# Kernel tuning notes

Measured on AMD Instinct MI355X. Metric: run time of the kernel, lower is better.

## Reference

```python
import jax, jax.numpy as jnp
import numpy as np

MIN = 1e-30
BLOCK = 64


def setup_inputs() -> dict:
    key = jax.random.key(0)
    ks = jax.random.split(key, 16)
    B, L, D, H, M, E, P, R = 4, 512, 768, 12, 48, 32, 512, 97
    inp = {
        "context": jax.random.normal(ks[0], (B, L, D), jnp.float32),
        "attention": jax.random.uniform(ks[1], (B, H, L, L), jnp.float32),
        "mention_map": jax.random.uniform(ks[2], (B, M, L), jnp.float32),
        "entity_map": jax.random.uniform(ks[3], (B, E, M), jnp.float32),
        "hts": jax.random.randint(ks[4], (B, P, 2), 0, E).astype(jnp.int64),
        "hW": jax.random.normal(ks[5], (D, D), jnp.float32) * 0.02,
        "hb": jnp.zeros((D,), jnp.float32),
        "tW": jax.random.normal(ks[6], (D, D), jnp.float32) * 0.02,
        "tb": jnp.zeros((D,), jnp.float32),
        "hcW": jax.random.normal(ks[7], (D, D), jnp.float32) * 0.02,
        "hcb": jnp.zeros((D,), jnp.float32),
        "tcW": jax.random.normal(ks[8], (D, D), jnp.float32) * 0.02,
        "tcb": jnp.zeros((D,), jnp.float32),
        "clasW": jax.random.normal(ks[9], (R, D * BLOCK), jnp.float32) * 0.02,
        "clasb": jnp.zeros((R,), jnp.float32),
    }
    return inp


def _group_bilinear(h, t, W, b):
    # h, t: [B, P, D]; grouped bilinear a la ATLOP: block-outer-product then linear
    B, P, D = h.shape
    nb = D // BLOCK
    h_ = h.reshape(B, P, nb, BLOCK)
    t_ = t.reshape(B, P, nb, BLOCK)
    feat = jnp.einsum("bpni,bpnj->bpnij", h_, t_).reshape(B, P, D * BLOCK)
    return feat @ W.T + b


def _forward(context, attention, mention_map, entity_map, hts,
             hW, hb, tW, tb, hcW, hcb, tcW, tcb, clasW, clasb):
    B = context.shape[0]
    bidx = jnp.arange(B)[:, None]
    h_idx = hts[..., 0]  # [B, P]
    t_idx = hts[..., 1]
    ht_mask = (hts.sum(-1) != 0)[..., None].astype(context.dtype)  # [B, P, 1]

    # ---- get_ht ----
    mention = mention_map @ context                       # [B, M, D]
    att_sum = attention.sum(axis=1)                       # [B, L, L]
    mention_att = mention_map @ att_sum @ jnp.swapaxes(mention_map, 1, 2)  # [B, M, M]
    entity_att = entity_map @ mention_att                 # [B, E, M]

    h_mask = entity_map[bidx, h_idx] * ht_mask            # [B, P, M]
    t_mask = entity_map[bidx, t_idx] * ht_mask
    h_att = entity_att[bidx, h_idx] * t_mask
    t_att = entity_att[bidx, t_idx] * h_mask
    h_att = h_att / (h_att.sum(-1, keepdims=True) + MIN)
    t_att = t_att / (t_att.sum(-1, keepdims=True) + MIN)
    h = (t_att @ mention) * ht_mask                       # [B, P, D]
    t = (h_att @ mention) * ht_mask

    # ---- context_pooling (entity_map projected to token space) ----
    em_tok = entity_map @ mention_map                     # [B, E, L]
    em_tok = em_tok / (em_tok.sum(-1, keepdims=True) + MIN)
    ent_att = jnp.einsum("bel,bhlm->bhem", em_tok, attention)  # [B, H, E, L]
    hA = ent_att[bidx, :, h_idx]                          # [B, P, H, L]
    tA = ent_att[bidx, :, t_idx]
    ctx_att = (hA * tA).sum(axis=2)                       # [B, P, L]
    ctx_att = ctx_att / (ctx_att.sum(-1, keepdims=True) + MIN)
    context_info = (ctx_att @ context) * ht_mask          # [B, P, D]

    h_info = context_info @ hcW.T + hcb
    t_info = context_info @ tcW.T + tcb
    h = jnp.tanh(h @ hW.T + hb + h_info)
    t = jnp.tanh(t @ tW.T + tb + t_info)
    return _group_bilinear(h, t, clasW, clasb)            # [B, P, R]


def reference(context, attention, mention_map, entity_map, hts,
              hW, hb, tW, tb, hcW, hcb, tcW, tcb, clasW, clasb):
    return _forward(context, attention, mention_map, entity_map, hts,
                    hW, hb, tW, tb, hcW, hcb, tcW, tcb, clasW, clasb)
```

## Files before the change

### kernel.cpp

```cpp
#include <hip/hip_runtime.h>
#include <math.h>

#define Bc 4
#define Lc 512
#define Dc 768
#define Hc 12
#define Mc 48
#define Ec 32
#define Pc 512
#define Rc 97
#define MINV 1e-30f
#define NSLICE 24

typedef _Float16 f16;
typedef __attribute__((ext_vector_type(8))) _Float16 f16x8;
typedef __attribute__((ext_vector_type(4))) _Float16 f16x4;
typedef __attribute__((ext_vector_type(16))) float f32x16;

__global__ __launch_bounds__(256) void k_prep(const float* __restrict__ ctx, f16* __restrict__ ctxT,
                                              const float* __restrict__ mm, f16* __restrict__ mmH,
                                              const float* __restrict__ em, f16* __restrict__ emtH,
                                              float* __restrict__ tmpML) {
    __shared__ f16 Ts[64][72];
    __shared__ float rowS[Mc];
    __shared__ float red[256];
    __shared__ float inv;
    int bid = blockIdx.x;
    int tid = threadIdx.x;
    if (bid < 384) {
        int id = bid;
        int dt = id % 12; int lt = (id / 12) % 8; int b = id / 96;
        int l0 = lt * 64, d0 = dt * 64;
        int r = tid >> 2, cg = tid & 3;
        const float* src = ctx + ((size_t)b * Lc + l0 + r) * Dc + d0 + cg * 16;
#pragma unroll
        for (int u = 0; u < 4; ++u) {
            float4 v = ((const float4*)src)[u];
            Ts[cg * 16 + u * 4 + 0][r] = (f16)v.x;
            Ts[cg * 16 + u * 4 + 1][r] = (f16)v.y;
            Ts[cg * 16 + u * 4 + 2][r] = (f16)v.z;
            Ts[cg * 16 + u * 4 + 3][r] = (f16)v.w;
        }
        __syncthreads();
        int dr = tid >> 2, seg = tid & 3;
        f16* dst = ctxT + ((size_t)b * Dc + d0 + dr) * Lc + l0 + seg * 16;
        f16x8 o0, o1;
#pragma unroll
        for (int j = 0; j < 8; ++j) { o0[j] = Ts[dr][seg * 16 + j]; o1[j] = Ts[dr][seg * 16 + 8 + j]; }
        *(f16x8*)dst = o0;
        *(f16x8*)(dst + 8) = o1;
    } else if (bid < 432) {
        int gid = (bid - 384) * 256 + tid;
        const float4* src = (const float4*)(mm + (size_t)gid * 8);
        float4 v0 = src[0], v1 = src[1];
        f16x8 o;
        o[0] = (f16)v0.x; o[1] = (f16)v0.y; o[2] = (f16)v0.z; o[3] = (f16)v0.w;
        o[4] = (f16)v1.x; o[5] = (f16)v1.y; o[6] = (f16)v1.z; o[7] = (f16)v1.w;
        ((f16x8*)mmH)[gid] = o;
    } else if (bid < 560) {
        int be = bid - 432; int b = be / Ec;
        if (tid < Mc) rowS[tid] = em[(size_t)be * Mc + tid];
        __syncthreads();
        float v0 = 0.f, v1 = 0.f;
        {
            const float* mb0 = mm + (size_t)b * Mc * Lc + tid;
            const float* mb1 = mm + (size_t)b * Mc * Lc + tid + 256;
            for (int m = 0; m < Mc; ++m) {
                v0 += rowS[m] * mb0[(size_t)m * Lc];
                v1 += rowS[m] * mb1[(size_t)m * Lc];
            }
        }
        red[tid] = v0 + v1;
        __syncthreads();
        for (int s = 128; s > 0; s >>= 1) { if (tid < s) red[tid] += red[tid + s]; __syncthreads(); }
        if (tid == 0) inv = 1.f / (red[0] + MINV);
        __syncthreads();
        emtH[(size_t)be * Lc + tid] = (f16)(v0 * inv);
        emtH[(size_t)be * Lc + tid + 256] = (f16)(v1 * inv);
    } else {
        int base = ((bid - 560) * 256 + tid) * 4;
        float4 z = make_float4(0.f, 0.f, 0.f, 0.f);
        float4* t4 = (float4*)tmpML;
#pragma unroll
        for (int u = 0; u < 4; ++u) t4[base + u] = z;
    }
}

__global__ __launch_bounds__(256) void k_att_mention(const f16* __restrict__ mmH,
                                                     const f16* __restrict__ emtH,
                                                     const float* __restrict__ att,
                                                     float* __restrict__ tmpML,
                                                     float* __restrict__ eat,
                                                     const f16* __restrict__ ctxT,
                                                     float* __restrict__ mention,
                                                     const float* __restrict__ hW, const float* __restrict__ tW,
                                                     const float* __restrict__ hcW, const float* __restrict__ tcW,
                                                     f16* __restrict__ hWb, f16* __restrict__ tWb,
                                                     f16* __restrict__ hcWb, f16* __restrict__ tcWb,
                                                     const float* __restrict__ clasW, f16* __restrict__ Wp) {
    __shared__ __align__(16) char smem[32768];
    int bid = blockIdx.x;
    int tid = threadIdx.x;
    int w = tid >> 6, lane = tid & 63;
    if (bid < 384) {
        f16* Ss   = (f16*)smem;
        f16* attS = (f16*)(smem + 12288);
        int mt = bid & 7; int bh = bid >> 3;
        int b = bh / Hc, h = bh % Hc;
        int m0 = mt * 64;
        int n_l = lane & 31, kg = lane >> 5;

        const float* ab = att + (size_t)bh * Lc * Lc + m0;
        int mRow = tid & 63, lg = tid >> 6;
        float pre[16];
#pragma unroll
        for (int q = 0; q < 16; ++q) pre[q] = ab[(size_t)(lg * 16 + q) * Lc + mRow];

        f32x16 acc[2];
#pragma unroll
        for (int nt = 0; nt < 2; ++nt)
#pragma unroll
            for (int i = 0; i < 16; ++i) acc[nt][i] = 0.f;

        for (int kc = 0; kc < 8; ++kc) {
            __syncthreads();
#pragma unroll
            for (int half = 0; half < 2; ++half) {
                int cc = lg * 2 + half;
                f16x8 v;
#pragma unroll
                for (int jj = 0; jj < 8; ++jj) v[jj] = (f16)pre[half * 8 + jj];
                ((f16x8*)attS)[mRow * 8 + (cc ^ (mRow & 7))] = v;
            }
#pragma unroll
            for (int k = 0; k < 3; ++k) {
                int idx = tid + k * 256;
                int row = idx >> 3, cc = idx & 7;
                f16x8 v;
                if (row < Mc) {
                    v = *(const f16x8*)(mmH + ((size_t)b * Mc + row) * Lc + kc * 64 + cc * 8);
                } else if (row < 80) {
                    v = *(const f16x8*)(emtH + ((size_t)b * Ec + row - Mc) * Lc + kc * 64 + cc * 8);
                } else {
#pragma unroll
                    for (int j = 0; j < 8; ++j) v[j] = (f16)0.f;
                }
                ((f16x8*)Ss)[row * 8 + (cc ^ (row & 7))] = v;
            }
            if (kc < 7) {
#pragma unroll
                for (int q = 0; q < 16; ++q)
                    pre[q] = ab[(size_t)((kc + 1) * 64 + lg * 16 + q) * Lc + mRow];
            }
            __syncthreads();
            if (w < 3) {
                int arow = w * 32 + n_l;
#pragma unroll
                for (int kk = 0; kk < 4; ++kk) {
                    int cc = kk * 2 + kg;
                    f16x8 a = ((const f16x8*)Ss)[arow * 8 + (cc ^ (arow & 7))];
#pragma unroll
                    for (int nt = 0; nt < 2; ++nt) {
                        int bcol = nt * 32 + n_l;
                        f16x8 bb = ((const f16x8*)attS)[bcol * 8 + (cc ^ (bcol & 7))];
                        acc[nt] = __builtin_amdgcn_mfma_f32_32x32x16_f16(a, bb, acc[nt], 0, 0, 0);
                    }
                }
            }
        }
        if (w < 3) {
#pragma unroll
            for (int nt = 0; nt < 2; ++nt)
#pragma unroll
                for (int reg = 0; reg < 16; ++reg) {
                    int row = (reg & 3) + 8 * (reg >> 2) + 4 * kg;
                    int rr = w * 32 + row;
                    int col = m0 + nt * 32 + n_l;
                    if (rr < Mc) {
                        atomicAdd(&tmpML[((size_t)b * Mc + rr) * Lc + col], acc[nt][reg]);
                    } else if (rr < 80) {
                        eat[(((size_t)b * Hc + h) * Ec + (rr - Mc)) * Lc + col] = acc[nt][reg];
                    }
                }
        }
    } else if (bid < 432) {
        f16* As = (f16*)smem;
        f16* Bs = (f16*)(smem + 16384);
        int id = bid - 384;
        int dt = id % 12; int b = id / 12;
        int d0 = dt * 64;
        int w_m = w & 1, w_n = w >> 1;
        int m_l = lane & 31, kg = lane >> 5;
        int r0 = tid >> 3, cc0 = tid & 7;
        int r1 = r0 + 32;
        int mr0 = (r0 < Mc) ? r0 : r0 - Mc;
        int mr1 = (r1 < Mc) ? r1 : r1 - Mc;
        f16x8 ar0, ar1, br0, br1;
        auto loadt = [&](int it) {
            int k0 = it * 64;
            ar0 = *(const f16x8*)(mmH + ((size_t)b * Mc + mr0) * Lc + k0 + cc0 * 8);
            ar1 = *(const f16x8*)(mmH + ((size_t)b * Mc + mr1) * Lc + k0 + cc0 * 8);
            br0 = *(const f16x8*)(ctxT + ((size_t)b * Dc + d0 + r0) * Lc + k0 + cc0 * 8);
            br1 = *(const f16x8*)(ctxT + ((size_t)b * Dc + d0 + r1) * Lc + k0 + cc0 * 8);
        };
        auto writet = [&](int p) {
            ((f16x8*)(As + p * 4096))[r0 * 8 + (cc0 ^ (r0 & 7))] = ar0;
            ((f16x8*)(As + p * 4096))[r1 * 8 + (cc0 ^ (r1 & 7))] = ar1;
            ((f16x8*)(Bs + p * 4096))[r0 * 8 + (cc0 ^ (r0 & 7))] = br0;
            ((f16x8*)(Bs + p * 4096))[r1 * 8 + (cc0 ^ (r1 & 7))] = br1;
        };
        loadt(0); writet(0); loadt(1);
        f32x16 acc;
#pragma unroll
        for (int i = 0; i < 16; ++i) acc[i] = 0.f;
        int ar = w_m * 32 + m_l;
        int br = w_n * 32 + m_l;
        for (int it = 0; it < 8; ++it) {
            int p = it & 1;
            __syncthreads();
            if (it < 7) writet(p ^ 1);
            if (it < 6) loadt(it + 2);
#pragma unroll
            for (int s = 0; s < 4; ++s) {
                int ck = s * 2 + kg;
                f16x8 a = ((const f16x8*)(As + p * 4096))[ar * 8 + (ck ^ (ar & 7))];
                f16x8 bv = ((const f16x8*)(Bs + p * 4096))[br * 8 + (ck ^ (br & 7))];
                acc = __builtin_amdgcn_mfma_f32_32x32x16_f16(a, bv, acc, 0, 0, 0);
            }
        }
#pragma unroll
        for (int reg = 0; reg < 16; ++reg) {
            int row = (reg & 3) + 8 * (reg >> 2) + 4 * kg;
            int m = w_m * 32 + row;
            if (m < Mc) mention[((size_t)b * Mc + m) * Dc + d0 + w_n * 32 + m_l] = acc[reg];
        }
    } else if (bid < 2480) {
        const int Q = 147456;
        int i = (bid - 432) * 256 + tid;
        int stride = 2048 * 256;
        for (; i < 4 * Q; i += stride) {
            int sel = i / Q, j = i % Q;
            const float* s = (sel == 0) ? hW : (sel == 1) ? tW : (sel == 2) ? hcW : tcW;
            f16* d = (sel == 0) ? hWb : (sel == 1) ? tWb : (sel == 2) ? hcWb : tcWb;
            float4 v = ((const float4*)s)[j];
            f16x4 o;
            o[0] = (f16)v.x; o[1] = (f16)v.y; o[2] = (f16)v.z; o[3] = (f16)v.w;
            ((f16x4*)d)[j] = o;
        }
    } else {
        f16 (*LsW)[72] = (f16 (*)[72])smem;
        int id2 = bid - 2480;
        int c = id2 >> 2, rt = id2 & 3;
        for (int idx = tid; idx < 512; idx += 256) {
            int row = idx >> 4, q = idx & 15;
            int r = rt * 32 + row;
            f16x4 o;
            if (r < Rc) {
                float4 v = *(const float4*)(clasW + (size_t)r * (Dc * 64) + c * 64 + q * 4);
                o[0] = (f16)v.x; o[1] = (f16)v.y; o[2] = (f16)v.z; o[3] = (f16)v.w;
            } else {
                o[0] = (f16)0.f; o[1] = (f16)0.f; o[2] = (f16)0.f; o[3] = (f16)0.f;
            }
            *(f16x4*)(&LsW[row][q * 4]) = o;
        }
        __syncthreads();
        int s = tid >> 6;
        int n_l = lane & 31, kg = lane >> 5;
        f16x8 outv = *(const f16x8*)(&LsW[n_l][s * 16 + kg * 8]);
        ((f16x8*)Wp)[(size_t)(c * 16 + s * 4 + rt) * 64 + lane] = outv;
    }
}

__global__ __launch_bounds__(256) void k_ma(const float* __restrict__ tmp,
                                            const float* __restrict__ mm,
                                            float* __restrict__ maS) {
    int wv = threadIdx.x >> 6, lane = threadIdx.x & 63;
    int gid = blockIdx.x * 4 + wv;
    int m2 = gid % 48;
    int m  = (gid / 48) % 48;
    int b  = gid / (48 * 48);
    const float4* t = (const float4*)(tmp + ((size_t)b * Mc + m)  * Lc);
    const float4* r = (const float4*)(mm  + ((size_t)b * Mc + m2) * Lc);
    float4 a0 = t[lane],      b0 = r[lane];
    float4 a1 = t[lane + 64], b1 = r[lane + 64];
    float acc = a0.x * b0.x + a0.y * b0.y + a0.z * b0.z + a0.w * b0.w
              + a1.x * b1.x + a1.y * b1.y + a1.z * b1.z + a1.w * b1.w;
#pragma unroll
    for (int off = 1; off < 64; off <<= 1) acc += __shfl_xor(acc, off);
    if (lane == 0) maS[gid] = acc;
}

__global__ __launch_bounds__(256) void k_pair(const int* __restrict__ hts,
                                              const float* __restrict__ em,
                                              const float* __restrict__ maS,
                                              const float* __restrict__ eat,
                                              f16* __restrict__ hatN, f16* __restrict__ tatN,
                                              f16* __restrict__ caH) {
    int wv = threadIdx.x >> 6, lane = threadIdx.x & 63;
    int bp = blockIdx.x * 4 + wv;
    int b = bp >> 9;
    int hi = hts[bp * 2], ti = hts[bp * 2 + 1];
    float mask = (hi + ti != 0) ? 1.f : 0.f;
    float hat = 0.f, tat = 0.f;
    if (lane < Mc) {
        float hm = em[((size_t)(b * Ec + hi)) * Mc + lane];
        float tm = em[((size_t)(b * Ec + ti)) * Mc + lane];
        float eh = 0.f, et = 0.f;
        const float* maB = maS + (size_t)b * Mc * Mc;
        const float* emH = em + ((size_t)(b * Ec + hi)) * Mc;
        const float* emT = em + ((size_t)(b * Ec + ti)) * Mc;
#pragma unroll 8
        for (int m = 0; m < Mc; ++m) {
            float ms = maB[m * Mc + lane];
            eh += emH[m] * ms;
            et += emT[m] * ms;
        }
        hat = eh * tm * mask;
        tat = et * hm * mask;
    }
    float sh = hat, st = tat;
#pragma unroll
    for (int off = 1; off < 64; off <<= 1) { sh += __shfl_xor(sh, off); st += __shfl_xor(st, off); }
    float hnorm = 1.f / (sh + MINV);
    float tnorm = 1.f / (st + MINV);
    hatN[(size_t)bp * 64 + lane] = (f16)(hat * hnorm);
    tatN[(size_t)bp * 64 + lane] = (f16)(tat * tnorm);

    const float* base = eat + (size_t)b * Hc * Ec * Lc;
    float prod[8];
    float tot = 0.f;
#pragma unroll
    for (int j8 = 0; j8 < 8; ++j8) {
        int j = j8 * 64 + lane;
        float a = 0.f;
#pragma unroll
        for (int h = 0; h < Hc; ++h)
            a += base[((size_t)h * Ec + hi) * Lc + j] * base[((size_t)h * Ec + ti) * Lc + j];
        prod[j8] = a;
        tot += a;
    }
#pragma unroll
    for (int off = 1; off < 64; off <<= 1) tot += __shfl_xor(tot, off);
    float inv = 1.f / (tot + MINV);
#pragma unroll
    for (int j8 = 0; j8 < 8; ++j8)
        caH[(size_t)bp * Lc + j8 * 64 + lane] = (f16)(prod[j8] * inv);
}

__global__ __launch_bounds__(256) void k_htci(const f16* __restrict__ tatN, const f16* __restrict__ hatN,
                                              const float* __restrict__ mention,
                                              f16* __restrict__ hB, f16* __restrict__ tB,
                                              const int* __restrict__ hts,
                                              const f16* __restrict__ caH,
                                              const f16* __restrict__ ctxT,
                                              f16* __restrict__ ci) {
    __shared__ __align__(16) char smem[33024];
    int bid = blockIdx.x;
    int tid = threadIdx.x;
    int w = tid >> 6, lane = tid & 63;
    int w_m = w & 1, w_n = w >> 1;
    int m_l = lane & 31, kg = lane >> 5;
    if (bid < 384) {
        f16* At = (f16*)smem;
        f16* Ah = (f16*)(smem + 8192);
        f16* Bs = (f16*)(smem + 16384);
        int m0 = (bid & 31) * 64;
        int b = m0 >> 9;
        int d0 = (bid >> 5) * 64;

        for (int i = tid; i < 512; i += 256) {
            int p = i >> 3, c = i & 7;
            ((f16x8*)At)[p * 8 + (c ^ (p & 7))] = *(const f16x8*)(tatN + (size_t)(m0 + p) * 64 + c * 8);
            ((f16x8*)Ah)[p * 8 + (c ^ (p & 7))] = *(const f16x8*)(hatN + (size_t)(m0 + p) * 64 + c * 8);
        }
        for (int i = tid; i < 512; i += 256) {
            f16x8 z;
#pragma unroll
            for (int j = 0; j < 8; ++j) z[j] = (f16)0.f;
            ((f16x8*)Bs)[i] = z;
        }
        __syncthreads();
        if (tid < 192) {
            int m = tid >> 2, q = tid & 3;
            const float4* src = (const float4*)(mention + ((size_t)b * Mc + m) * Dc + d0 + q * 16);
#pragma unroll
            for (int u = 0; u < 4; ++u) {
                float4 v = src[u];
                int dl = q * 16 + u * 4;
#pragma unroll
                for (int x = 0; x < 4; ++x) {
                    float vv = (x == 0) ? v.x : (x == 1) ? v.y : (x == 2) ? v.z : v.w;
                    int d = dl + x;
                    Bs[(d * 8 + ((m >> 3) ^ (d & 7))) * 8 + (m & 7)] = (f16)vv;
                }
            }
        }
        __syncthreads();

        f32x16 acch, acct;
#pragma unroll
        for (int i = 0; i < 16; ++i) { acch[i] = 0.f; acct[i] = 0.f; }
        int ar = w_m * 32 + m_l;
        int br = w_n * 32 + m_l;
#pragma unroll
        for (int s = 0; s < 4; ++s) {
            int ck = s * 2 + kg;
            f16x8 at_ = ((const f16x8*)At)[ar * 8 + (ck ^ (ar & 7))];
            f16x8 ah_ = ((const f16x8*)Ah)[ar * 8 + (ck ^ (ar & 7))];
            f16x8 bv = ((const f16x8*)Bs)[br * 8 + (ck ^ (br & 7))];
            acch = __builtin_amdgcn_mfma_f32_32x32x16_f16(at_, bv, acch, 0, 0, 0);
            acct = __builtin_amdgcn_mfma_f32_32x32x16_f16(ah_, bv, acct, 0, 0, 0);
        }
#pragma unroll
        for (int reg = 0; reg < 16; ++reg) {
            int row = (reg & 3) + 8 * (reg >> 2) + 4 * kg;
            int p = m0 + w_m * 32 + row;
            int d = d0 + w_n * 32 + m_l;
            hB[(size_t)p * Dc + d] = (f16)acch[reg];
            tB[(size_t)p * Dc + d] = (f16)acct[reg];
        }
    } else {
        f16* As = (f16*)smem;
        f16* Bs = (f16*)(smem + 16384);
        float* maskS = (float*)(smem + 32768);
        int id = bid - 384;
        int dt = id % 12; int pt = (id / 12) % 8; int b = id / 96;
        int p0 = pt * 64, d0 = dt * 64;
        int r0 = tid >> 3, cc0 = tid & 7;
        int r1 = r0 + 32;
        if (tid < 64) {
            int bp = b * Pc + p0 + tid;
            maskS[tid] = (hts[bp * 2] + hts[bp * 2 + 1] != 0) ? 1.f : 0.f;
        }
        f16x8 ar0, ar1, br0, br1;
        auto loadt = [&](int it) {
            int k0 = it * 64;
            ar0 = *(const f16x8*)(caH + (size_t)(b * Pc + p0 + r0) * Lc + k0 + cc0 * 8);
            ar1 = *(const f16x8*)(caH + (size_t)(b * Pc + p0 + r1) * Lc + k0 + cc0 * 8);
            br0 = *(const f16x8*)(ctxT + (size_t)(b * Dc + d0 + r0) * Lc + k0 + cc0 * 8);
            br1 = *(const f16x8*)(ctxT + (size_t)(b * Dc + d0 + r1) * Lc + k0 + cc0 * 8);
        };
        auto writet = [&](int p) {
            ((f16x8*)(As + p * 4096))[r0 * 8 + (cc0 ^ (r0 & 7))] = ar0;
            ((f16x8*)(As + p * 4096))[r1 * 8 + (cc0 ^ (r1 & 7))] = ar1;
            ((f16x8*)(Bs + p * 4096))[r0 * 8 + (cc0 ^ (r0 & 7))] = br0;
            ((f16x8*)(Bs + p * 4096))[r1 * 8 + (cc0 ^ (r1 & 7))] = br1;
        };
        loadt(0); writet(0); loadt(1);
        f32x16 acc;
#pragma unroll
        for (int i = 0; i < 16; ++i) acc[i] = 0.f;
        int ar = w_m * 32 + m_l;
        int br = w_n * 32 + m_l;
        for (int it = 0; it < 8; ++it) {
            int p = it & 1;
            __syncthreads();
            if (it < 7) writet(p ^ 1);
            if (it < 6) loadt(it + 2);
#pragma unroll
            for (int s = 0; s < 4; ++s) {
                int ck = s * 2 + kg;
                f16x8 a = ((const f16x8*)(As + p * 4096))[ar * 8 + (ck ^ (ar & 7))];
                f16x8 bv = ((const f16x8*)(Bs + p * 4096))[br * 8 + (ck ^ (br & 7))];
                acc = __builtin_amdgcn_mfma_f32_32x32x16_f16(a, bv, acc, 0, 0, 0);
            }
        }
#pragma unroll
        for (int reg = 0; reg < 16; ++reg) {
            int row = (reg & 3) + 8 * (reg >> 2) + 4 * kg;
            int p = p0 + w_m * 32 + row;
            int d = d0 + w_n * 32 + m_l;
            ci[(size_t)(b * Pc + p) * Dc + d] = (f16)(acc[reg] * maskS[w_m * 32 + row]);
        }
    }
}

__global__ __launch_bounds__(256) void k_proj_mfma(const f16* __restrict__ Xh, const f16* __restrict__ Wh,
                                                   const float* __restrict__ bh,
                                                   const f16* __restrict__ Xt, const f16* __restrict__ Wt,
                                                   const float* __restrict__ bt,
                                                   const f16* __restrict__ Xc, const f16* __restrict__ Whc,
                                                   const float* __restrict__ bhc,
                                                   const f16* __restrict__ Wtc, const float* __restrict__ btc,
                                                   f16* __restrict__ outh, f16* __restrict__ outt) {
    __shared__ __align__(16) f16 Xs[2][64 * 64];
    __shared__ __align__(16) f16 Ws[2][64 * 64];
    int z = blockIdx.z;
    const f16* X1 = z ? Xt : Xh;
    const f16* W1 = z ? Wt : Wh;
    const float* b1 = z ? bt : bh;
    const f16* W2 = z ? Wtc : Whc;
    const float* b2 = z ? btc : bhc;
    f16* outp = z ? outt : outh;
    int m0 = blockIdx.x * 64, n0 = blockIdx.y * 64;
    int tid = threadIdx.x;
    int w = tid >> 6, lane = tid & 63;
    int w_m = w & 1, w_n = w >> 1;
    int m_l = lane & 31, kg = lane >> 5;
    const f16* Xarr[2] = {X1, Xc};
    const f16* Warr[2] = {W1, W2};

    auto stage = [&](int p, int it) {
        int src = it / 12; int k0 = (it % 12) * 64;
        const f16* X = Xarr[src]; const f16* W = Warr[src];
#pragma unroll
        for (int g = 0; g < 2; ++g) {
            int s = g * 256 + w * 64 + lane;
            int r = s >> 3, c = (s & 7) ^ (r & 7);
            __builtin_amdgcn_global_load_lds(
                (const __attribute__((address_space(1))) void*)(X + (size_t)(m0 + r) * Dc + k0 + c * 8),
                (__attribute__((address_space(3))) void*)(&Xs[p][(g * 256 + w * 64) * 8]),
                16, 0, 0);
            __builtin_amdgcn_global_load_lds(
                (const __attribute__((address_space(1))) void*)(W + (size_t)(n0 + r) * Dc + k0 + c * 8),
                (__attribute__((address_space(3))) void*)(&Ws[p][(g * 256 + w * 64) * 8]),
                16, 0, 0);
        }
    };

    stage(0, 0);
    f32x16 acc;
#pragma unroll
    for (int i = 0; i < 16; ++i) acc[i] = 0.f;
    int ar = w_m * 32 + m_l;
    int br = w_n * 32 + m_l;
    for (int it = 0; it < 24; ++it) {
        int p = it & 1;
        __syncthreads();
        if (it < 23) stage(p ^ 1, it + 1);
#pragma unroll
        for (int s = 0; s < 4; ++s) {
            int ck = s * 2 + kg;
            f16x8 a = ((const f16x8*)Xs[p])[ar * 8 + (ck ^ (ar & 7))];
            f16x8 b = ((const f16x8*)Ws[p])[br * 8 + (ck ^ (br & 7))];
            acc = __builtin_amdgcn_mfma_f32_32x32x16_f16(a, b, acc, 0, 0, 0);
        }
    }
#pragma unroll
    for (int reg = 0; reg < 16; ++reg) {
        int row = (reg & 3) + 8 * (reg >> 2) + 4 * kg;
        int m = m0 + w_m * 32 + row;
        int n = n0 + w_n * 32 + m_l;
        float v = tanhf(acc[reg] + b1[n] + b2[n]);
        outp[(size_t)m * Dc + n] = (f16)v;
    }
}

__global__ __launch_bounds__(256, 3) void k_bilin(const f16* __restrict__ hF, const f16* __restrict__ tF,
                                                  const f16* __restrict__ Wp, f16* __restrict__ partial) {
    __shared__ __align__(16) f16 tS[128 * 64];
    __shared__ f16 hS[128 * 33];
    int id = blockIdx.x;
    int rh = id & 1;
    int st = id >> 1;
    int slice = st % NSLICE;
    int tile = st / NSLICE;
    int bp0 = tile * 128;
    int c0 = slice * 32;
    int n = c0 >> 6;
    int tid = threadIdx.x;
    int w = tid >> 6, lane = tid & 63;
    int w_m = w & 1, w_r = w >> 1;
    int m_l = lane & 31, kg = lane >> 5;
    int rt = rh * 2 + w_r;

    for (int idx = tid; idx < 128 * 4; idx += 256) {
        int bp = idx >> 2, seg = idx & 3;
        f16x8 hv = *(const f16x8*)(hF + (size_t)(bp0 + bp) * Dc + c0 + seg * 8);
#pragma unroll
        for (int j = 0; j < 8; ++j) hS[bp * 33 + seg * 8 + j] = hv[j];
    }
    for (int idx = tid; idx < 128 * 8; idx += 256) {
        int bp = idx >> 3, cc = idx & 7;
        f16x8 tv = *(const f16x8*)(tF + (size_t)(bp0 + bp) * Dc + n * 64 + cc * 8);
        ((f16x8*)tS)[bp * 8 + (cc ^ (bp & 7))] = tv;
    }
    __syncthreads();

    int rowA = w_m * 64 + m_l;
    int rowB = rowA + 32;

    f16x8 tvA[4], tvB[4];
#pragma unroll
    for (int s = 0; s < 4; ++s) {
        int ck = s * 2 + kg;
        tvA[s] = ((const f16x8*)tS)[rowA * 8 + (ck ^ (rowA & 7))];
        tvB[s] = ((const f16x8*)tS)[rowB * 8 + (ck ^ (rowB & 7))];
    }

    f32x16 acc[2];
#pragma unroll
    for (int mt = 0; mt < 2; ++mt)
#pragma unroll
        for (int i = 0; i < 16; ++i) acc[mt][i] = 0.f;

    const f16x8* wpb = (const f16x8*)Wp + ((size_t)c0 * 16 + rt) * 64 + lane;
    f16x8 BfA[4], BfB[4];
#pragma unroll
    for (int s = 0; s < 4; ++s) BfA[s] = wpb[s * 256];

    for (int io = 0; io < 32; io += 2) {
#pragma unroll
        for (int s = 0; s < 4; ++s) BfB[s] = wpb[(io + 1) * 1024 + s * 256];
        {
            f16 hv0 = hS[rowA * 33 + io];
            f16 hv1 = hS[rowB * 33 + io];
#pragma unroll
            for (int s = 0; s < 4; ++s) {
                f16x8 a0 = tvA[s] * hv0;
                f16x8 a1 = tvB[s] * hv1;
                acc[0] = __builtin_amdgcn_mfma_f32_32x32x16_f16(a0, BfA[s], acc[0], 0, 0, 0);
                acc[1] = __builtin_amdgcn_mfma_f32_32x32x16_f16(a1, BfA[s], acc[1], 0, 0, 0);
            }
        }
        if (io + 2 < 32) {
#pragma unroll
            for (int s = 0; s < 4; ++s) BfA[s] = wpb[(io + 2) * 1024 + s * 256];
        }
        {
            f16 hv0 = hS[rowA * 33 + io + 1];
            f16 hv1 = hS[rowB * 33 + io + 1];
#pragma unroll
            for (int s = 0; s < 4; ++s) {
                f16x8 a0 = tvA[s] * hv0;
                f16x8 a1 = tvB[s] * hv1;
                acc[0] = __builtin_amdgcn_mfma_f32_32x32x16_f16(a0, BfB[s], acc[0], 0, 0, 0);
                acc[1] = __builtin_amdgcn_mfma_f32_32x32x16_f16(a1, BfB[s], acc[1], 0, 0, 0);
            }
        }
    }

    f16* pbase = partial + (size_t)slice * (2048 * 128);
    int r = rt * 32 + m_l;
#pragma unroll
    for (int mt = 0; mt < 2; ++mt)
#pragma unroll
        for (int reg = 0; reg < 16; ++reg) {
            int row = (reg & 3) + 8 * (reg >> 2) + 4 * kg;
            int bp = bp0 + w_m * 64 + mt * 32 + row;
            pbase[(size_t)bp * 128 + r] = (f16)acc[mt][reg];
        }
}

__global__ __launch_bounds__(256) void k_reduce(const f16* __restrict__ partial,
                                                const float* __restrict__ cb,
                                                float* __restrict__ out) {
    int idx = blockIdx.x * 256 + threadIdx.x;
    int bp = idx >> 5, c = idx & 31;
    const f16x4* p = (const f16x4*)partial + idx;
    float a0 = 0.f, a1 = 0.f, a2 = 0.f, a3 = 0.f;
#pragma unroll
    for (int s = 0; s < NSLICE; ++s) {
        f16x4 v = p[(size_t)s * (2048 * 32)];
        a0 += (float)v[0]; a1 += (float)v[1]; a2 += (float)v[2]; a3 += (float)v[3];
    }
    int rb = c * 4;
    float* ob = out + (size_t)bp * Rc;
    if (rb + 0 < Rc) ob[rb + 0] = a0 + cb[rb + 0];
    if (rb + 1 < Rc) ob[rb + 1] = a1 + cb[rb + 1];
    if (rb + 2 < Rc) ob[rb + 2] = a2 + cb[rb + 2];
    if (rb + 3 < Rc) ob[rb + 3] = a3 + cb[rb + 3];
}

extern "C" void kernel_launch(void* const* d_in, const int* in_sizes, int n_in,
                              void* d_out, int out_size, void* d_ws, size_t ws_size,
                              hipStream_t stream) {
    const float* context   = (const float*)d_in[0];
    const float* attention = (const float*)d_in[1];
    const float* mm        = (const float*)d_in[2];
    const float* em        = (const float*)d_in[3];
    const int*   hts       = (const int*)d_in[4];
    const float* hW        = (const float*)d_in[5];
    const float* hb        = (const float*)d_in[6];
    const float* tW        = (const float*)d_in[7];
    const float* tb        = (const float*)d_in[8];
    const float* hcW       = (const float*)d_in[9];
    const float* hcb       = (const float*)d_in[10];
    const float* tcW       = (const float*)d_in[11];
    const float* tcb       = (const float*)d_in[12];
    const float* clasW     = (const float*)d_in[13];
    const float* clasb     = (const float*)d_in[14];
    float* out = (float*)d_out;

    char* wsb = (char*)d_ws;
    auto alloc = [&](size_t bytes) { char* p = wsb; wsb += (bytes + 255) & ~(size_t)255; return p; };
    float* mention     = (float*)alloc((size_t)Bc * Mc * Dc * 4);
    float* tmpML       = (float*)alloc((size_t)Bc * Mc * Lc * 4);
    float* ent_att     = (float*)alloc((size_t)Bc * Hc * Ec * Lc * 4);
    float* maS         = (float*)alloc((size_t)Bc * Mc * Mc * 4);
    f16* em_tok  = (f16*)alloc((size_t)Bc * Ec * Lc * 2);
    f16* ctx_att = (f16*)alloc((size_t)Bc * Pc * Lc * 2);
    f16* mmH     = (f16*)alloc((size_t)Bc * Mc * Lc * 2);
    f16* hatN    = (f16*)alloc((size_t)Bc * Pc * 64 * 2);
    f16* tatN    = (f16*)alloc((size_t)Bc * Pc * 64 * 2);
    f16* h_buf   = (f16*)alloc((size_t)Bc * Pc * Dc * 2);
    f16* t_buf   = (f16*)alloc((size_t)Bc * Pc * Dc * 2);
    f16* ctxinfo = (f16*)alloc((size_t)Bc * Pc * Dc * 2);
    f16* h_fin   = (f16*)alloc((size_t)Bc * Pc * Dc * 2);
    f16* t_fin   = (f16*)alloc((size_t)Bc * Pc * Dc * 2);
    f16* hWb     = (f16*)alloc((size_t)Dc * Dc * 2);
    f16* tWb     = (f16*)alloc((size_t)Dc * Dc * 2);
    f16* hcWb    = (f16*)alloc((size_t)Dc * Dc * 2);
    f16* tcWb    = (f16*)alloc((size_t)Dc * Dc * 2);
    f16* ctxT    = (f16*)alloc((size_t)Bc * Dc * Lc * 2);
    f16* Wp      = (f16*)alloc((size_t)768 * 16 * 64 * 8 * 2);
    f16* partial = (f16*)alloc((size_t)NSLICE * 2048 * 128 * 2);

    k_prep<<<dim3(584), dim3(256), 0, stream>>>(context, ctxT, mm, mmH, em, em_tok, tmpML);
    k_att_mention<<<dim3(5552), dim3(256), 0, stream>>>(mmH, em_tok, attention, tmpML, ent_att,
                                                        ctxT, mention,
                                                        hW, tW, hcW, tcW, hWb, tWb, hcWb, tcWb,
                                                        clasW, Wp);
    k_ma<<<dim3(Bc * Mc * Mc / 4), dim3(256), 0, stream>>>(tmpML, mm, maS);
    k_pair<<<dim3(Bc * Pc / 4), dim3(256), 0, stream>>>(hts, em, maS, ent_att, hatN, tatN, ctx_att);
    k_htci<<<dim3(768), dim3(256), 0, stream>>>(tatN, hatN, mention, h_buf, t_buf,
                                                hts, ctx_att, ctxT, ctxinfo);
    k_proj_mfma<<<dim3(32, 12, 2), dim3(256), 0, stream>>>(h_buf, hWb, hb, t_buf, tWb, tb,
                                                           ctxinfo, hcWb, hcb, tcWb, tcb, h_fin, t_fin);
    k_bilin<<<dim3(16 * NSLICE * 2), dim3(256), 0, stream>>>(h_fin, t_fin, Wp, partial);
    k_reduce<<<dim3(256), dim3(256), 0, stream>>>(partial, clasb, out);
}
```

Baseline: 244.0 us.

## Reassociate h/t projection: premultiply mention by weights before pair attention

Applies the linear layers hW and tW to the 48 mentions per batch (mention @ W^T) in extra blocks of k_ma, instead of to the 2048 pair vectors. k_htci then multiplies the pair attention weights by these premultiplied mention matrices and writes fp32 pre-activations. k_proj_mfma now only does the context-info projection (K=768 instead of 1536) and adds the precomputed term before tanh. This cuts GEMM FLOPs in the projection, at the cost of writing and reading two fp32 [2048x768] buffers and changing rounding order.

```diff
diff --git a/kernel.cpp b/kernel.cpp
--- a/kernel.cpp
+++ b/kernel.cpp
@@ -273,21 +273,98 @@
 
 __global__ __launch_bounds__(256) void k_ma(const float* __restrict__ tmp,
                                             const float* __restrict__ mm,
-                                            float* __restrict__ maS) {
-    int wv = threadIdx.x >> 6, lane = threadIdx.x & 63;
-    int gid = blockIdx.x * 4 + wv;
-    int m2 = gid % 48;
-    int m  = (gid / 48) % 48;
-    int b  = gid / (48 * 48);
-    const float4* t = (const float4*)(tmp + ((size_t)b * Mc + m)  * Lc);
-    const float4* r = (const float4*)(mm  + ((size_t)b * Mc + m2) * Lc);
-    float4 a0 = t[lane],      b0 = r[lane];
-    float4 a1 = t[lane + 64], b1 = r[lane + 64];
-    float acc = a0.x * b0.x + a0.y * b0.y + a0.z * b0.z + a0.w * b0.w
-              + a1.x * b1.x + a1.y * b1.y + a1.z * b1.z + a1.w * b1.w;
-#pragma unroll
-    for (int off = 1; off < 64; off <<= 1) acc += __shfl_xor(acc, off);
-    if (lane == 0) maS[gid] = acc;
+                                            float* __restrict__ maS,
+                                            const float* __restrict__ mention,
+                                            const f16* __restrict__ hWb, const f16* __restrict__ tWb,
+                                            f16* __restrict__ menWT) {
+    __shared__ __align__(16) f16 As[2][64 * 64];
+    __shared__ __align__(16) f16 Bs[2][64 * 64];
+    int bid = blockIdx.x;
+    int tid = threadIdx.x;
+    if (bid < 2304) {
+        int wv = tid >> 6, lane = tid & 63;
+        int gid = bid * 4 + wv;
+        int m2 = gid % 48;
+        int m  = (gid / 48) % 48;
+        int b  = gid / (48 * 48);
+        const float4* t = (const float4*)(tmp + ((size_t)b * Mc + m)  * Lc);
+        const float4* r = (const float4*)(mm  + ((size_t)b * Mc + m2) * Lc);
+        float4 a0 = t[lane],      b0 = r[lane];
+        float4 a1 = t[lane + 64], b1 = r[lane + 64];
+        float acc = a0.x * b0.x + a0.y * b0.y + a0.z * b0.z + a0.w * b0.w
+                  + a1.x * b1.x + a1.y * b1.y + a1.z * b1.z + a1.w * b1.w;
+#pragma unroll
+        for (int off = 1; off < 64; off <<= 1) acc += __shfl_xor(acc, off);
+        if (lane == 0) maS[gid] = acc;
+    } else {
+        int id2 = bid - 2304;
+        int b = id2 / 24;
+        int rem = id2 % 24;
+        int z = rem / 12;
+        int dt = rem % 12;
+        int d0 = dt * 64;
+        const f16* Wz = z ? tWb : hWb;
+        int w = tid >> 6, lane = tid & 63;
+        int w_m = w & 1, w_n = w >> 1;
+        int m_l = lane & 31, kg = lane >> 5;
+        int r0 = tid >> 3, cc0 = tid & 7;
+        int r1 = r0 + 32;
+        f16x8 ar0, ar1, br0, br1;
+        auto loadt = [&](int it) {
+            int k0 = it * 64;
+            if (r0 < Mc) {
+                const float* A0 = mention + ((size_t)b * Mc + r0) * Dc + k0 + cc0 * 8;
+#pragma unroll
+                for (int j = 0; j < 8; ++j) ar0[j] = (f16)A0[j];
+            } else {
+#pragma unroll
+                for (int j = 0; j < 8; ++j) ar0[j] = (f16)0.f;
+            }
+            if (r1 < Mc) {
+                const float* A1 = mention + ((size_t)b * Mc + r1) * Dc + k0 + cc0 * 8;
+#pragma unroll
+                for (int j = 0; j < 8; ++j) ar1[j] = (f16)A1[j];
+            } else {
+#pragma unroll
+                for (int j = 0; j < 8; ++j) ar1[j] = (f16)0.f;
+            }
+            br0 = *(const f16x8*)(Wz + (size_t)(d0 + r0) * Dc + k0 + cc0 * 8);
+            br1 = *(const f16x8*)(Wz + (size_t)(d0 + r1) * Dc + k0 + cc0 * 8);
+        };
+        auto writet = [&](int p) {
+            ((f16x8*)As[p])[r0 * 8 + (cc0 ^ (r0 & 7))] = ar0;
+            ((f16x8*)As[p])[r1 * 8 + (cc0 ^ (r1 & 7))] = ar1;
+            ((f16x8*)Bs[p])[r0 * 8 + (cc0 ^ (r0 & 7))] = br0;
+            ((f16x8*)Bs[p])[r1 * 8 + (cc0 ^ (r1 & 7))] = br1;
+        };
+        loadt(0); writet(0); loadt(1);
+        f32x16 acc;
+#pragma unroll
+        for (int i = 0; i < 16; ++i) acc[i] = 0.f;
+        int ar = w_m * 32 + m_l;
+        int br = w_n * 32 + m_l;
+        for (int it = 0; it < 12; ++it) {
+            int p = it & 1;
+            __syncthreads();
+            if (it < 11) writet(p ^ 1);
+            if (it < 10) loadt(it + 2);
+#pragma unroll
+            for (int s = 0; s < 4; ++s) {
+                int ck = s * 2 + kg;
+                f16x8 a = ((const f16x8*)As[p])[ar * 8 + (ck ^ (ar & 7))];
+                f16x8 bv = ((const f16x8*)Bs[p])[br * 8 + (ck ^ (br & 7))];
+                acc = __builtin_amdgcn_mfma_f32_32x32x16_f16(a, bv, acc, 0, 0, 0);
+            }
+        }
+        f16* base = menWT + (size_t)(b * 2 + z) * Dc * 64;
+#pragma unroll
+        for (int reg = 0; reg < 16; ++reg) {
+            int row = (reg & 3) + 8 * (reg >> 2) + 4 * kg;
+            int m_out = w_m * 32 + row;
+            int d_out = d0 + w_n * 32 + m_l;
+            base[(size_t)d_out * 64 + m_out] = (f16)acc[reg];
+        }
+    }
 }
 
 __global__ __launch_bounds__(256) void k_pair(const int* __restrict__ hts,
@@ -348,8 +425,8 @@
 }
 
 __global__ __launch_bounds__(256) void k_htci(const f16* __restrict__ tatN, const f16* __restrict__ hatN,
-                                              const float* __restrict__ mention,
-                                              f16* __restrict__ hB, f16* __restrict__ tB,
+                                              const f16* __restrict__ menWT,
+                                              float* __restrict__ hB2, float* __restrict__ tB2,
                                               const int* __restrict__ hts,
                                               const f16* __restrict__ caH,
                                               const f16* __restrict__ ctxT,
@@ -363,37 +440,20 @@
     if (bid < 384) {
         f16* At = (f16*)smem;
         f16* Ah = (f16*)(smem + 8192);
-        f16* Bs = (f16*)(smem + 16384);
+        f16* Bh = (f16*)(smem + 16384);
+        f16* Bt = (f16*)(smem + 24576);
         int m0 = (bid & 31) * 64;
         int b = m0 >> 9;
         int d0 = (bid >> 5) * 64;
+        const f16* mh = menWT + (size_t)(b * 2 + 0) * Dc * 64 + (size_t)d0 * 64;
+        const f16* mt = menWT + (size_t)(b * 2 + 1) * Dc * 64 + (size_t)d0 * 64;
 
         for (int i = tid; i < 512; i += 256) {
             int p = i >> 3, c = i & 7;
             ((f16x8*)At)[p * 8 + (c ^ (p & 7))] = *(const f16x8*)(tatN + (size_t)(m0 + p) * 64 + c * 8);
             ((f16x8*)Ah)[p * 8 + (c ^ (p & 7))] = *(const f16x8*)(hatN + (size_t)(m0 + p) * 64 + c * 8);
-        }
-        for (int i = tid; i < 512; i += 256) {
-            f16x8 z;
-#pragma unroll
-            for (int j = 0; j < 8; ++j) z[j] = (f16)0.f;
-            ((f16x8*)Bs)[i] = z;
-        }
-        __syncthreads();
-        if (tid < 192) {
-            int m = tid >> 2, q = tid & 3;
-            const float4* src = (const float4*)(mention + ((size_t)b * Mc + m) * Dc + d0 + q * 16);
-#pragma unroll
-            for (int u = 0; u < 4; ++u) {
-                float4 v = src[u];
-                int dl = q * 16 + u * 4;
-#pragma unroll
-                for (int x = 0; x < 4; ++x) {
-                    float vv = (x == 0) ? v.x : (x == 1) ? v.y : (x == 2) ? v.z : v.w;
-                    int d = dl + x;
-                    Bs[(d * 8 + ((m >> 3) ^ (d & 7))) * 8 + (m & 7)] = (f16)vv;
-                }
-            }
+            ((f16x8*)Bh)[p * 8 + (c ^ (p & 7))] = *(const f16x8*)(mh + (size_t)p * 64 + c * 8);
+            ((f16x8*)Bt)[p * 8 + (c ^ (p & 7))] = *(const f16x8*)(mt + (size_t)p * 64 + c * 8);
         }
         __syncthreads();
 
@@ -407,17 +467,18 @@
             int ck = s * 2 + kg;
             f16x8 at_ = ((const f16x8*)At)[ar * 8 + (ck ^ (ar & 7))];
             f16x8 ah_ = ((const f16x8*)Ah)[ar * 8 + (ck ^ (ar & 7))];
-            f16x8 bv = ((const f16x8*)Bs)[br * 8 + (ck ^ (br & 7))];
-            acch = __builtin_amdgcn_mfma_f32_32x32x16_f16(at_, bv, acch, 0, 0, 0);
-            acct = __builtin_amdgcn_mfma_f32_32x32x16_f16(ah_, bv, acct, 0, 0, 0);
+            f16x8 bvh = ((const f16x8*)Bh)[br * 8 + (ck ^ (br & 7))];
+            f16x8 bvt = ((const f16x8*)Bt)[br * 8 + (ck ^ (br & 7))];
+            acch = __builtin_amdgcn_mfma_f32_32x32x16_f16(at_, bvh, acch, 0, 0, 0);
+            acct = __builtin_amdgcn_mfma_f32_32x32x16_f16(ah_, bvt, acct, 0, 0, 0);
         }
 #pragma unroll
         for (int reg = 0; reg < 16; ++reg) {
             int row = (reg & 3) + 8 * (reg >> 2) + 4 * kg;
             int p = m0 + w_m * 32 + row;
             int d = d0 + w_n * 32 + m_l;
-            hB[(size_t)p * Dc + d] = (f16)acch[reg];
-            tB[(size_t)p * Dc + d] = (f16)acct[reg];
+            hB2[(size_t)p * Dc + d] = acch[reg];
+            tB2[(size_t)p * Dc + d] = acct[reg];
         }
     } else {
         f16* As = (f16*)smem;
@@ -475,44 +536,39 @@
     }
 }
 
-__global__ __launch_bounds__(256) void k_proj_mfma(const f16* __restrict__ Xh, const f16* __restrict__ Wh,
-                                                   const float* __restrict__ bh,
-                                                   const f16* __restrict__ Xt, const f16* __restrict__ Wt,
+__global__ __launch_bounds__(256) void k_proj_mfma(const float* __restrict__ bh,
                                                    const float* __restrict__ bt,
                                                    const f16* __restrict__ Xc, const f16* __restrict__ Whc,
                                                    const float* __restrict__ bhc,
                                                    const f16* __restrict__ Wtc, const float* __restrict__ btc,
+                                                   const float* __restrict__ hB2, const float* __restrict__ tB2,
                                                    f16* __restrict__ outh, f16* __restrict__ outt) {
     __shared__ __align__(16) f16 Xs[2][64 * 64];
     __shared__ __align__(16) f16 Ws[2][64 * 64];
     int z = blockIdx.z;
-    const f16* X1 = z ? Xt : Xh;
-    const f16* W1 = z ? Wt : Wh;
     const float* b1 = z ? bt : bh;
     const f16* W2 = z ? Wtc : Whc;
     const float* b2 = z ? btc : bhc;
+    const float* HB2 = z ? tB2 : hB2;
     f16* outp = z ? outt : outh;
     int m0 = blockIdx.x * 64, n0 = blockIdx.y * 64;
     int tid = threadIdx.x;
     int w = tid >> 6, lane = tid & 63;
     int w_m = w & 1, w_n = w >> 1;
     int m_l = lane & 31, kg = lane >> 5;
-    const f16* Xarr[2] = {X1, Xc};
-    const f16* Warr[2] = {W1, W2};
 
     auto stage = [&](int p, int it) {
-        int src = it / 12; int k0 = (it % 12) * 64;
-        const f16* X = Xarr[src]; const f16* W = Warr[src];
+        int k0 = it * 64;
 #pragma unroll
         for (int g = 0; g < 2; ++g) {
             int s = g * 256 + w * 64 + lane;
             int r = s >> 3, c = (s & 7) ^ (r & 7);
             __builtin_amdgcn_global_load_lds(
-                (const __attribute__((address_space(1))) void*)(X + (size_t)(m0 + r) * Dc + k0 + c * 8),
+                (const __attribute__((address_space(1))) void*)(Xc + (size_t)(m0 + r) * Dc + k0 + c * 8),
                 (__attribute__((address_space(3))) void*)(&Xs[p][(g * 256 + w * 64) * 8]),
                 16, 0, 0);
             __builtin_amdgcn_global_load_lds(
-                (const __attribute__((address_space(1))) void*)(W + (size_t)(n0 + r) * Dc + k0 + c * 8),
+                (const __attribute__((address_space(1))) void*)(W2 + (size_t)(n0 + r) * Dc + k0 + c * 8),
                 (__attribute__((address_space(3))) void*)(&Ws[p][(g * 256 + w * 64) * 8]),
                 16, 0, 0);
         }
@@ -524,10 +580,10 @@
     for (int i = 0; i < 16; ++i) acc[i] = 0.f;
     int ar = w_m * 32 + m_l;
     int br = w_n * 32 + m_l;
-    for (int it = 0; it < 24; ++it) {
+    for (int it = 0; it < 12; ++it) {
         int p = it & 1;
         __syncthreads();
-        if (it < 23) stage(p ^ 1, it + 1);
+        if (it < 11) stage(p ^ 1, it + 1);
 #pragma unroll
         for (int s = 0; s < 4; ++s) {
             int ck = s * 2 + kg;
@@ -541,7 +597,7 @@
         int row = (reg & 3) + 8 * (reg >> 2) + 4 * kg;
         int m = m0 + w_m * 32 + row;
         int n = n0 + w_n * 32 + m_l;
-        float v = tanhf(acc[reg] + b1[n] + b2[n]);
+        float v = tanhf(acc[reg] + HB2[(size_t)m * Dc + n] + b1[n] + b2[n]);
         outp[(size_t)m * Dc + n] = (f16)v;
     }
 }
@@ -688,13 +744,14 @@
     float* tmpML       = (float*)alloc((size_t)Bc * Mc * Lc * 4);
     float* ent_att     = (float*)alloc((size_t)Bc * Hc * Ec * Lc * 4);
     float* maS         = (float*)alloc((size_t)Bc * Mc * Mc * 4);
+    float* hB2         = (float*)alloc((size_t)Bc * Pc * Dc * 4);
+    float* tB2         = (float*)alloc((size_t)Bc * Pc * Dc * 4);
     f16* em_tok  = (f16*)alloc((size_t)Bc * Ec * Lc * 2);
     f16* ctx_att = (f16*)alloc((size_t)Bc * Pc * Lc * 2);
     f16* mmH     = (f16*)alloc((size_t)Bc * Mc * Lc * 2);
     f16* hatN    = (f16*)alloc((size_t)Bc * Pc * 64 * 2);
     f16* tatN    = (f16*)alloc((size_t)Bc * Pc * 64 * 2);
-    f16* h_buf   = (f16*)alloc((size_t)Bc * Pc * Dc * 2);
-    f16* t_buf   = (f16*)alloc((size_t)Bc * Pc * Dc * 2);
+    f16* menWT   = (f16*)alloc((size_t)Bc * 2 * Dc * 64 * 2);
     f16* ctxinfo = (f16*)alloc((size_t)Bc * Pc * Dc * 2);
     f16* h_fin   = (f16*)alloc((size_t)Bc * Pc * Dc * 2);
     f16* t_fin   = (f16*)alloc((size_t)Bc * Pc * Dc * 2);
@@ -711,12 +768,12 @@
                                                         ctxT, mention,
                                                         hW, tW, hcW, tcW, hWb, tWb, hcWb, tcWb,
                                                         clasW, Wp);
-    k_ma<<<dim3(Bc * Mc * Mc / 4), dim3(256), 0, stream>>>(tmpML, mm, maS);
+    k_ma<<<dim3(2400), dim3(256), 0, stream>>>(tmpML, mm, maS, mention, hWb, tWb, menWT);
     k_pair<<<dim3(Bc * Pc / 4), dim3(256), 0, stream>>>(hts, em, maS, ent_att, hatN, tatN, ctx_att);
-    k_htci<<<dim3(768), dim3(256), 0, stream>>>(tatN, hatN, mention, h_buf, t_buf,
+    k_htci<<<dim3(768), dim3(256), 0, stream>>>(tatN, hatN, menWT, hB2, tB2,
                                                 hts, ctx_att, ctxT, ctxinfo);
-    k_proj_mfma<<<dim3(32, 12, 2), dim3(256), 0, stream>>>(h_buf, hWb, hb, t_buf, tWb, tb,
-                                                           ctxinfo, hcWb, hcb, tcWb, tcb, h_fin, t_fin);
+    k_proj_mfma<<<dim3(32, 12, 2), dim3(256), 0, stream>>>(hb, tb, ctxinfo, hcWb, hcb, tcWb, tcb,
+                                                           hB2, tB2, h_fin, t_fin);
     k_bilin<<<dim3(16 * NSLICE * 2), dim3(256), 0, stream>>>(h_fin, t_fin, Wp, partial);
     k_reduce<<<dim3(256), dim3(256), 0, stream>>>(partial, clasb, out);
 }
```

After: 251.5 us. +3.1%, slower.

## Split bilinear K across warp halves and halve partial slices

Applied to the files above, without the earlier changes.

Each bilinear block now covers a 64-wide h slice (a whole 64-block) and handles one 32-row output tile. The two warp halves split the K range and combine their accumulators through shared memory before writing fp16 partials. This halves the number of partial slices written and later summed by the reduce kernel, and it loads each t tile once per 64 h columns instead of once per 32. The grid keeps the same block count, and the cost is an extra shared-memory reduction with two barriers per block.

```diff
diff --git a/kernel.cpp b/kernel.cpp
--- a/kernel.cpp
+++ b/kernel.cpp
@@ -10,7 +10,7 @@
 #define Pc 512
 #define Rc 97
 #define MINV 1e-30f
-#define NSLICE 24
+#define NSLICE 12
 
 typedef _Float16 f16;
 typedef __attribute__((ext_vector_type(8))) _Float16 f16x8;
@@ -549,26 +549,25 @@
 __global__ __launch_bounds__(256, 3) void k_bilin(const f16* __restrict__ hF, const f16* __restrict__ tF,
                                                   const f16* __restrict__ Wp, f16* __restrict__ partial) {
     __shared__ __align__(16) f16 tS[128 * 64];
-    __shared__ f16 hS[128 * 33];
+    __shared__ f16 hS[128 * 65];
     int id = blockIdx.x;
-    int rh = id & 1;
-    int st = id >> 1;
+    int rt = id & 3;
+    int st = id >> 2;
     int slice = st % NSLICE;
     int tile = st / NSLICE;
     int bp0 = tile * 128;
-    int c0 = slice * 32;
-    int n = c0 >> 6;
+    int c0 = slice * 64;
+    int n = slice;
     int tid = threadIdx.x;
     int w = tid >> 6, lane = tid & 63;
-    int w_m = w & 1, w_r = w >> 1;
+    int w_m = w & 1, w_half = w >> 1;
     int m_l = lane & 31, kg = lane >> 5;
-    int rt = rh * 2 + w_r;
-
-    for (int idx = tid; idx < 128 * 4; idx += 256) {
-        int bp = idx >> 2, seg = idx & 3;
+
+    for (int idx = tid; idx < 128 * 8; idx += 256) {
+        int bp = idx >> 3, seg = idx & 7;
         f16x8 hv = *(const f16x8*)(hF + (size_t)(bp0 + bp) * Dc + c0 + seg * 8);
 #pragma unroll
-        for (int j = 0; j < 8; ++j) hS[bp * 33 + seg * 8 + j] = hv[j];
+        for (int j = 0; j < 8; ++j) hS[bp * 65 + seg * 8 + j] = hv[j];
     }
     for (int idx = tid; idx < 128 * 8; idx += 256) {
         int bp = idx >> 3, cc = idx & 7;
@@ -594,7 +593,8 @@
 #pragma unroll
         for (int i = 0; i < 16; ++i) acc[mt][i] = 0.f;
 
-    const f16x8* wpb = (const f16x8*)Wp + ((size_t)c0 * 16 + rt) * 64 + lane;
+    const f16x8* wpb = (const f16x8*)Wp + ((size_t)(c0 + w_half * 32) * 16 + rt) * 64 + lane;
+    int hbase = w_half * 32;
     f16x8 BfA[4], BfB[4];
 #pragma unroll
     for (int s = 0; s < 4; ++s) BfA[s] = wpb[s * 256];
@@ -603,8 +603,8 @@
 #pragma unroll
         for (int s = 0; s < 4; ++s) BfB[s] = wpb[(io + 1) * 1024 + s * 256];
         {
-            f16 hv0 = hS[rowA * 33 + io];
-            f16 hv1 = hS[rowB * 33 + io];
+            f16 hv0 = hS[rowA * 65 + hbase + io];
+            f16 hv1 = hS[rowB * 65 + hbase + io];
 #pragma unroll
             for (int s = 0; s < 4; ++s) {
                 f16x8 a0 = tvA[s] * hv0;
@@ -618,8 +618,8 @@
             for (int s = 0; s < 4; ++s) BfA[s] = wpb[(io + 2) * 1024 + s * 256];
         }
         {
-            f16 hv0 = hS[rowA * 33 + io + 1];
-            f16 hv1 = hS[rowB * 33 + io + 1];
+            f16 hv0 = hS[rowA * 65 + hbase + io + 1];
+            f16 hv1 = hS[rowB * 65 + hbase + io + 1];
 #pragma unroll
             for (int s = 0; s < 4; ++s) {
                 f16x8 a0 = tvA[s] * hv0;
@@ -630,16 +630,29 @@
         }
     }
 
-    f16* pbase = partial + (size_t)slice * (2048 * 128);
-    int r = rt * 32 + m_l;
-#pragma unroll
-    for (int mt = 0; mt < 2; ++mt)
-#pragma unroll
-        for (int reg = 0; reg < 16; ++reg) {
-            int row = (reg & 3) + 8 * (reg >> 2) + 4 * kg;
-            int bp = bp0 + w_m * 64 + mt * 32 + row;
-            pbase[(size_t)bp * 128 + r] = (f16)acc[mt][reg];
-        }
+    float* comb = (float*)tS;
+    __syncthreads();
+    if (w_half == 1) {
+#pragma unroll
+        for (int mt = 0; mt < 2; ++mt)
+#pragma unroll
+            for (int reg = 0; reg < 16; ++reg)
+                comb[((w_m * 2 + mt) * 16 + reg) * 64 + lane] = acc[mt][reg];
+    }
+    __syncthreads();
+    if (w_half == 0) {
+        f16* pbase = partial + (size_t)slice * (2048 * 128);
+        int r = rt * 32 + m_l;
+#pragma unroll
+        for (int mt = 0; mt < 2; ++mt)
+#pragma unroll
+            for (int reg = 0; reg < 16; ++reg) {
+                float v = acc[mt][reg] + comb[((w_m * 2 + mt) * 16 + reg) * 64 + lane];
+                int row = (reg & 3) + 8 * (reg >> 2) + 4 * kg;
+                int bp = bp0 + w_m * 64 + mt * 32 + row;
+                pbase[(size_t)bp * 128 + r] = (f16)v;
+            }
+    }
 }
 
 __global__ __launch_bounds__(256) void k_reduce(const f16* __restrict__ partial,
@@ -717,6 +730,6 @@
                                                 hts, ctx_att, ctxT, ctxinfo);
     k_proj_mfma<<<dim3(32, 12, 2), dim3(256), 0, stream>>>(h_buf, hWb, hb, t_buf, tWb, tb,
                                                            ctxinfo, hcWb, hcb, tcWb, tcb, h_fin, t_fin);
-    k_bilin<<<dim3(16 * NSLICE * 2), dim3(256), 0, stream>>>(h_fin, t_fin, Wp, partial);
+    k_bilin<<<dim3(16 * NSLICE * 4), dim3(256), 0, stream>>>(h_fin, t_fin, Wp, partial);
     k_reduce<<<dim3(256), dim3(256), 0, stream>>>(partial, clasb, out);
 }
```

Measured after the change: 242.4 us. Within noise of the previous version (-0.7%).
